# Kernel optimization log

Hardware: AMD Instinct MI355X
Metric: run time of the kernel (lower is better)

The kernel has to match this reference:

```python
import jax, jax.numpy as jnp
import numpy as np

N = 100000          # nodes per node type (paper, author)
E = 250000          # edges per relation
D_IN = 128          # input feature dim
H, C = 4, 32        # heads, channels per head (h_dim = H*C = 128)
HD = H * C
OUT = 349           # num classes
RELS = ["c", "w", "wb"]  # cites(paper->paper), writes(author->paper), written_by(paper->author)


def setup_inputs() -> dict:
    key = jax.random.key(0)
    ks = iter(jax.random.split(key, 64))
    def nrm(shape, scale=0.1):
        return jax.random.normal(next(ks), shape, jnp.float32) * scale
    inp = {
        "x_paper": jax.random.normal(next(ks), (N, D_IN), jnp.float32),
        "x_author": jax.random.normal(next(ks), (N, D_IN), jnp.float32),
        "ei_cites": jax.random.randint(next(ks), (2, E), 0, N),
        "ei_writes": jax.random.randint(next(ks), (2, E), 0, N),
        "ei_written": jax.random.randint(next(ks), (2, E), 0, N),
    }
    for l, din in [(0, D_IN), (1, HD)]:
        for r in RELS:
            inp[f"W{l}_{r}"] = nrm((din, HD))
            inp[f"as{l}_{r}"] = nrm((H, C))
            inp[f"ad{l}_{r}"] = nrm((H, C))
            inp[f"b{l}_{r}"] = jnp.zeros((HD,), jnp.float32)
    inp["lin_W"] = nrm((HD, OUT))
    inp["lin_b"] = jnp.zeros((OUT,), jnp.float32)
    return inp


def _gat_conv(x_src, x_dst, ei, W, att_s, att_d, b, n_dst):
    """PyG GATConv (concat heads, add_self_loops=False, shared lin for src/dst)."""
    h_s = (x_src @ W).reshape(-1, H, C)              # [Ns,H,C]
    h_d = (x_dst @ W).reshape(-1, H, C)              # [Nd,H,C]
    a_s = (h_s * att_s).sum(-1)                      # [Ns,H]
    a_d = (h_d * att_d).sum(-1)                      # [Nd,H]
    src, dst = ei[0], ei[1]
    e = jax.nn.leaky_relu(a_s[src] + a_d[dst], 0.2)  # [E,H]
    # segment softmax over incoming edges per dst node
    m = jax.ops.segment_max(e, dst, num_segments=n_dst)
    m = jnp.where(jnp.isfinite(m), m, 0.0)
    w = jnp.exp(e - m[dst])
    z = jax.ops.segment_sum(w, dst, num_segments=n_dst)
    alpha = w / (z[dst] + 1e-16)                     # [E,H]
    msg = h_s[src] * alpha[..., None]                # [E,H,C]
    agg = jax.ops.segment_sum(msg, dst, num_segments=n_dst)
    return agg.reshape(n_dst, HD) + b


def _forward(x_paper, x_author, ei_cites, ei_writes, ei_written, params, lin_W, lin_b):
    xp, xa = x_paper, x_author
    for l in range(2):
        p = params[l]
        # HeteroConv with sum aggregation across relations per dst node type
        op = _gat_conv(xp, xp, ei_cites, *p["c"], N) + _gat_conv(xa, xp, ei_writes, *p["w"], N)
        oa = _gat_conv(xp, xa, ei_written, *p["wb"], N)
        xp, xa = op, oa
        if l != 1:
            xp = jax.nn.leaky_relu(xp, 0.01)  # F.leaky_relu default slope
            xa = jax.nn.leaky_relu(xa, 0.01)
            # dropout: identity in eval/reference mode
    return xp @ lin_W + lin_b  # [N, OUT]


def reference(x_paper, x_author,
              W0_c, as0_c, ad0_c, b0_c, W0_w, as0_w, ad0_w, b0_w, W0_wb, as0_wb, ad0_wb, b0_wb,
              W1_c, as1_c, ad1_c, b1_c, W1_w, as1_w, ad1_w, b1_w, W1_wb, as1_wb, ad1_wb, b1_wb,
              lin_W, lin_b, ei_cites, ei_writes, ei_written):
    params = [
        {"c": (W0_c, as0_c, ad0_c, b0_c), "w": (W0_w, as0_w, ad0_w, b0_w), "wb": (W0_wb, as0_wb, ad0_wb, b0_wb)},
        {"c": (W1_c, as1_c, ad1_c, b1_c), "w": (W1_w, as1_w, ad1_w, b1_w), "wb": (W1_wb, as1_wb, ad1_wb, b1_wb)},
    ]
    return _forward(x_paper, x_author, ei_cites, ei_writes, ei_written, params, lin_W, lin_b)
```

## Files before the change

kernel.cpp:

```cpp
#include <hip/hip_runtime.h>

#define NN 100000
#define EE 250000
#define CAP 32

typedef unsigned int u32;
typedef unsigned short ushort;
typedef __attribute__((ext_vector_type(8))) short bf16x8;
typedef __attribute__((ext_vector_type(4))) float f32x4;

__device__ __forceinline__ ushort f2bf(float x) {
    u32 u = __float_as_uint(x);
    return (ushort)((u + 0x7fffu + ((u >> 16) & 1u)) >> 16);
}
__device__ __forceinline__ float bf2f(ushort h) {
    return __uint_as_float(((u32)h) << 16);
}

__global__ __launch_bounds__(256) void gemm_att(
    const float* __restrict__ X, const float* __restrict__ W,
    const float* __restrict__ atts, const float* __restrict__ attd,
    float* __restrict__ H, float* __restrict__ aS, float* __restrict__ aD)
{
    __shared__ float sW[64 * 128];
    __shared__ float sXT[128 * 32];
    const int tid = threadIdx.x;
    const size_t r0 = (size_t)blockIdx.x * 32;

    {
        int rl = tid & 31, kg = tid >> 5;
        const float4* Xr = (const float4*)(X + (r0 + rl) * 128);
#pragma unroll
        for (int t = 0; t < 4; ++t) {
            float4 u = Xr[kg * 4 + t];
            int k = kg * 16 + t * 4;
            sXT[(k + 0) * 32 + rl] = u.x;
            sXT[(k + 1) * 32 + rl] = u.y;
            sXT[(k + 2) * 32 + rl] = u.z;
            sXT[(k + 3) * 32 + rl] = u.w;
        }
    }

    const int jg = tid & 31;
    const int rg = tid >> 5;
    float acc[4][4] = {};

    for (int kh = 0; kh < 2; ++kh) {
        __syncthreads();
        const float4* Wu = (const float4*)(W + kh * 64 * 128);
        float4* sWv = (float4*)sW;
#pragma unroll
        for (int t = 0; t < 8; ++t)
            sWv[tid + 256 * t] = Wu[tid + 256 * t];
        __syncthreads();
#pragma unroll 4
        for (int k = 0; k < 64; ++k) {
            const float4 w = ((const float4*)sW)[k * 32 + jg];
            const int kk = kh * 64 + k;
            const float4 x = ((const float4*)sXT)[kk * 8 + rg];
            acc[0][0] += w.x * x.x; acc[0][1] += w.y * x.x; acc[0][2] += w.z * x.x; acc[0][3] += w.w * x.x;
            acc[1][0] += w.x * x.y; acc[1][1] += w.y * x.y; acc[1][2] += w.z * x.y; acc[1][3] += w.w * x.y;
            acc[2][0] += w.x * x.z; acc[2][1] += w.y * x.z; acc[2][2] += w.z * x.z; acc[2][3] += w.w * x.z;
            acc[3][0] += w.x * x.w; acc[3][1] += w.y * x.w; acc[3][2] += w.z * x.w; acc[3][3] += w.w * x.w;
        }
    }

    const float4 sv = ((const float4*)atts)[jg];
    const float4 dv = ((const float4*)attd)[jg];
    const int h = jg >> 3;

#pragma unroll
    for (int i = 0; i < 4; ++i) {
        const size_t row = r0 + rg * 4 + i;
        if (H)
            ((float4*)H)[row * 32 + jg] = make_float4(acc[i][0], acc[i][1], acc[i][2], acc[i][3]);
        float ps = acc[i][0] * sv.x + acc[i][1] * sv.y + acc[i][2] * sv.z + acc[i][3] * sv.w;
        float pd = acc[i][0] * dv.x + acc[i][1] * dv.y + acc[i][2] * dv.z + acc[i][3] * dv.w;
        ps += __shfl_xor(ps, 1); ps += __shfl_xor(ps, 2); ps += __shfl_xor(ps, 4);
        pd += __shfl_xor(pd, 1); pd += __shfl_xor(pd, 2); pd += __shfl_xor(pd, 4);
        if ((jg & 7) == 0) {
            aS[row * 4 + h] = ps;
            aD[row * 4 + h] = pd;
        }
    }
}

__global__ __launch_bounds__(256) void fold_w3(
    const float* __restrict__ W0, const float* __restrict__ a0,
    const float* __restrict__ W1, const float* __restrict__ a1,
    const float* __restrict__ W2, const float* __restrict__ a2,
    float* __restrict__ Wf)
{
    int i = blockIdx.x * 256 + threadIdx.x;
    if (i >= 1536) return;
    int r = i >> 9, j = i & 511;
    int k = j >> 2, h = j & 3;
    const float* W = (r == 0) ? W0 : (r == 1) ? W1 : W2;
    const float* a = (r == 0) ? a0 : (r == 1) ? a1 : a2;
    float s = 0.f;
#pragma unroll
    for (int c = 0; c < 32; ++c)
        s += W[k * 128 + h * 32 + c] * a[h * 32 + c];
    Wf[i] = s;
}

__global__ __launch_bounds__(256) void gemv_att(
    const float* __restrict__ X, const float* __restrict__ Wf,
    float* __restrict__ aD)
{
    __shared__ float sWf[512];
    const int tid = threadIdx.x;
    if (tid < 128)
        ((float4*)sWf)[tid] = ((const float4*)Wf)[tid];
    __syncthreads();
    const int t = blockIdx.x * 256 + tid;
    const int n = t >> 5, lane = t & 31;
    if (n >= NN) return;
    const float4 x = ((const float4*)X)[(size_t)n * 32 + lane];
    const float4 w0 = ((const float4*)sWf)[lane * 4 + 0];
    const float4 w1 = ((const float4*)sWf)[lane * 4 + 1];
    const float4 w2 = ((const float4*)sWf)[lane * 4 + 2];
    const float4 w3 = ((const float4*)sWf)[lane * 4 + 3];
    float p0 = x.x * w0.x + x.y * w1.x + x.z * w2.x + x.w * w3.x;
    float p1 = x.x * w0.y + x.y * w1.y + x.z * w2.y + x.w * w3.y;
    float p2 = x.x * w0.z + x.y * w1.z + x.z * w2.z + x.w * w3.z;
    float p3 = x.x * w0.w + x.y * w1.w + x.z * w2.w + x.w * w3.w;
#pragma unroll
    for (int off = 1; off < 32; off <<= 1) {
        p0 += __shfl_xor(p0, off);
        p1 += __shfl_xor(p1, off);
        p2 += __shfl_xor(p2, off);
        p3 += __shfl_xor(p3, off);
    }
    if (lane == 0)
        ((float4*)aD)[n] = make_float4(p0, p1, p2, p3);
}

__global__ __launch_bounds__(256) void fill_buckets(
    const int* __restrict__ ei, int* __restrict__ deg, int* __restrict__ bkt)
{
    int e = blockIdx.x * 256 + threadIdx.x;
    if (e >= EE) return;
    int s = ei[e], d = ei[EE + e];
    int slot = atomicAdd(&deg[d], 1);
    if (slot >= 0 && slot < CAP) bkt[(size_t)d * CAP + slot] = s;
}

__device__ __forceinline__ float4 agg_one(
    int d, int lane, int h,
    const int* __restrict__ deg, const int* __restrict__ bkt,
    const float* __restrict__ aS, const float* __restrict__ aD,
    const float* __restrict__ Hs)
{
    int g = deg[d]; if (g > CAP) g = CAP; if (g < 0) g = 0;
    const float adh = aD[d * 4 + h];
    const int* mybkt = bkt + (size_t)d * CAP;

    const int4 sa = *(const int4*)mybkt;
    const int4 sb = *(const int4*)(mybkt + 4);
    int sidx[8] = {sa.x, sa.y, sa.z, sa.w, sb.x, sb.y, sb.z, sb.w};
#pragma unroll
    for (int j = 0; j < 8; ++j)
        sidx[j] = (j < g) ? sidx[j] : 0;

    float e[8];
#pragma unroll
    for (int j = 0; j < 8; ++j) {
        float ev = aS[sidx[j] * 4 + h] + adh;
        e[j] = ev > 0.f ? ev : 0.2f * ev;
    }
    float m = -INFINITY;
#pragma unroll
    for (int j = 0; j < 8; ++j)
        if (j < g) m = fmaxf(m, e[j]);
    for (int j = 8; j < g; ++j) {
        int s = mybkt[j];
        float ev = aS[s * 4 + h] + adh;
        ev = ev > 0.f ? ev : 0.2f * ev;
        m = fmaxf(m, ev);
    }

    float4 acc = make_float4(0.f, 0.f, 0.f, 0.f);
    float z = 0.f;
#pragma unroll
    for (int j = 0; j < 8; ++j) {
        if (j < g) {
            float w = __expf(e[j] - m);
            z += w;
            float4 hv = ((const float4*)Hs)[(size_t)sidx[j] * 32 + lane];
            acc.x += w * hv.x; acc.y += w * hv.y; acc.z += w * hv.z; acc.w += w * hv.w;
        }
    }
    for (int j = 8; j < g; ++j) {
        int s = mybkt[j];
        float ev = aS[s * 4 + h] + adh;
        ev = ev > 0.f ? ev : 0.2f * ev;
        float w = __expf(ev - m);
        z += w;
        float4 hv = ((const float4*)Hs)[(size_t)s * 32 + lane];
        acc.x += w * hv.x; acc.y += w * hv.y; acc.z += w * hv.z; acc.w += w * hv.w;
    }
    float inv = 1.f / (z + 1e-16f);
    acc.x *= inv; acc.y *= inv; acc.z *= inv; acc.w *= inv;
    return acc;
}

__global__ __launch_bounds__(256) void aggregate(
    const int* __restrict__ deg, const int* __restrict__ bkt,
    const float* __restrict__ aS, const float* __restrict__ aD,
    const float* __restrict__ Hs, float* __restrict__ out,
    const float* __restrict__ b1, int act)
{
    int t = blockIdx.x * 256 + threadIdx.x;
    int d = t >> 5, lane = t & 31;
    if (d >= NN) return;
    const int h = lane >> 3;
    float4 acc = agg_one(d, lane, h, deg, bkt, aS, aD, Hs);
    if (b1) {
        float4 bv = ((const float4*)b1)[lane];
        acc.x += bv.x; acc.y += bv.y; acc.z += bv.z; acc.w += bv.w;
    }
    if (act) {
        acc.x = acc.x > 0.f ? acc.x : 0.01f * acc.x;
        acc.y = acc.y > 0.f ? acc.y : 0.01f * acc.y;
        acc.z = acc.z > 0.f ? acc.z : 0.01f * acc.z;
        acc.w = acc.w > 0.f ? acc.w : 0.01f * acc.w;
    }
    ((float4*)out)[(size_t)d * 32 + lane] = acc;
}

__global__ __launch_bounds__(256) void aggregate2(
    const int* __restrict__ deg_c, const int* __restrict__ bkt_c,
    const float* __restrict__ aS_c, const float* __restrict__ aD_c,
    const float* __restrict__ Hs_c,
    const int* __restrict__ deg_w, const int* __restrict__ bkt_w,
    const float* __restrict__ aS_w, const float* __restrict__ aD_w,
    const float* __restrict__ Hs_w,
    float* __restrict__ out,
    const float* __restrict__ b1, const float* __restrict__ b2, int act)
{
    int t = blockIdx.x * 256 + threadIdx.x;
    int d = t >> 5, lane = t & 31;
    if (d >= NN) return;
    const int h = lane >> 3;
    float4 acc_c = agg_one(d, lane, h, deg_c, bkt_c, aS_c, aD_c, Hs_c);
    float4 acc  = agg_one(d, lane, h, deg_w, bkt_w, aS_w, aD_w, Hs_w);
    acc.x += acc_c.x; acc.y += acc_c.y; acc.z += acc_c.z; acc.w += acc_c.w;
    {
        float4 bv = ((const float4*)b1)[lane];
        acc.x += bv.x; acc.y += bv.y; acc.z += bv.z; acc.w += bv.w;
    }
    {
        float4 bv = ((const float4*)b2)[lane];
        acc.x += bv.x; acc.y += bv.y; acc.z += bv.z; acc.w += bv.w;
    }
    if (act) {
        acc.x = acc.x > 0.f ? acc.x : 0.01f * acc.x;
        acc.y = acc.y > 0.f ? acc.y : 0.01f * acc.y;
        acc.z = acc.z > 0.f ? acc.z : 0.01f * acc.z;
        acc.w = acc.w > 0.f ? acc.w : 0.01f * acc.w;
    }
    ((float4*)out)[(size_t)d * 32 + lane] = acc;
}

__global__ __launch_bounds__(256) void pad_w(
    const float* __restrict__ Wl, const float* __restrict__ bl,
    ushort* __restrict__ Whi, ushort* __restrict__ Wlo, float* __restrict__ bp)
{
    int i = blockIdx.x * 256 + threadIdx.x;
    if (i >= 384 * 128) return;
    int n = i >> 7, k = i & 127;
    float w = (n < 349) ? Wl[k * 349 + n] : 0.0f;
    ushort h = f2bf(w);
    Whi[i] = h;
    Wlo[i] = f2bf(w - bf2f(h));
    if (i < 384) bp[i] = (i < 349) ? bl[i] : 0.0f;
}

__global__ __launch_bounds__(256) void gemm_out(
    const float* __restrict__ X, const ushort* __restrict__ Whi,
    const ushort* __restrict__ Wlo, const float* __restrict__ bp,
    float* __restrict__ out)
{
    __shared__ __align__(16) char smem[22400];
    ushort* sAhi = (ushort*)smem;
    ushort* sAlo = (ushort*)(smem + 8192);
    float*  sOut = (float*)smem;
    const int tid = threadIdx.x;
    const size_t r0 = (size_t)blockIdx.x * 32;

    {
        const int rl = tid >> 3, sub = tid & 7;
        const float4* Xr = (const float4*)(X + (r0 + rl) * 128);
        const u32 swz = ((u32)(rl & 7)) << 4;
#pragma unroll
        for (int i = 0; i < 2; ++i) {
            float4 u0 = Xr[sub * 4 + 2 * i];
            float4 u1 = Xr[sub * 4 + 2 * i + 1];
            float v[8] = {u0.x, u0.y, u0.z, u0.w, u1.x, u1.y, u1.z, u1.w};
            bf16x8 h8, l8;
#pragma unroll
            for (int e = 0; e < 8; ++e) {
                ushort h = f2bf(v[e]);
                h8[e] = (short)h;
                l8[e] = (short)f2bf(v[e] - bf2f(h));
            }
            u32 byteoff = (((u32)rl * 256u) + (u32)(sub * 32 + i * 16)) ^ swz;
            *(bf16x8*)((char*)sAhi + byteoff) = h8;
            *(bf16x8*)((char*)sAlo + byteoff) = l8;
        }
    }
    __syncthreads();

    const int wave = tid >> 6, lane = tid & 63;
    const int lr = lane & 15;
    const int lg = lane >> 4;
    const int ncol0 = wave * 96;

    f32x4 acc[2][6];
#pragma unroll
    for (int mt = 0; mt < 2; ++mt)
#pragma unroll
        for (int nt = 0; nt < 6; ++nt)
            acc[mt][nt] = (f32x4){0.f, 0.f, 0.f, 0.f};

    for (int ks = 0; ks < 4; ++ks) {
        bf16x8 ah[2], al[2];
#pragma unroll
        for (int mt = 0; mt < 2; ++mt) {
            const int row = mt * 16 + lr;
            u32 byteoff = (((u32)row * 256u) + (u32)(ks * 64 + lg * 16))
                          ^ (((u32)(row & 7)) << 4);
            ah[mt] = *(const bf16x8*)((const char*)sAhi + byteoff);
            al[mt] = *(const bf16x8*)((const char*)sAlo + byteoff);
        }
#pragma unroll
        for (int nt = 0; nt < 6; ++nt) {
            const int n = ncol0 + nt * 16 + lr;
            const size_t off = (size_t)n * 128 + ks * 32 + lg * 8;
            const bf16x8 bh = *(const bf16x8*)(Whi + off);
            const bf16x8 bl = *(const bf16x8*)(Wlo + off);
#pragma unroll
            for (int mt = 0; mt < 2; ++mt) {
                acc[mt][nt] = __builtin_amdgcn_mfma_f32_16x16x32_bf16(
                    ah[mt], bh, acc[mt][nt], 0, 0, 0);
                acc[mt][nt] = __builtin_amdgcn_mfma_f32_16x16x32_bf16(
                    ah[mt], bl, acc[mt][nt], 0, 0, 0);
                acc[mt][nt] = __builtin_amdgcn_mfma_f32_16x16x32_bf16(
                    al[mt], bh, acc[mt][nt], 0, 0, 0);
            }
        }
    }
    __syncthreads();

    for (int mt = 0; mt < 2; ++mt) {
        if (mt) __syncthreads();
#pragma unroll
        for (int nt = 0; nt < 6; ++nt) {
            const int n = ncol0 + nt * 16 + lr;
            if (n < 349) {
                const float bb = bp[n];
#pragma unroll
                for (int r = 0; r < 4; ++r)
                    sOut[(lg * 4 + r) * 349 + n] = acc[mt][nt][r] + bb;
            }
        }
        __syncthreads();
        {
            float4* dst = (float4*)(out + (r0 + (size_t)mt * 16) * 349);
            const float4* src = (const float4*)sOut;
            for (int i = tid; i < 1396; i += 256)
                dst[i] = src[i];
        }
    }
}

extern "C" void kernel_launch(void* const* d_in, const int* in_sizes, int n_in,
                              void* d_out, int out_size, void* d_ws, size_t ws_size,
                              hipStream_t stream)
{
    (void)in_sizes; (void)n_in; (void)out_size; (void)ws_size;
    const float* xp = (const float*)d_in[0];
    const float* xa = (const float*)d_in[1];
    const int* eic = (const int*)d_in[2];
    const int* eiw = (const int*)d_in[3];
    const int* eiwb = (const int*)d_in[4];
    auto Wl = [&](int l, int r) { return (const float*)d_in[5 + (l * 3 + r) * 4 + 0]; };
    auto As = [&](int l, int r) { return (const float*)d_in[5 + (l * 3 + r) * 4 + 1]; };
    auto Ad = [&](int l, int r) { return (const float*)d_in[5 + (l * 3 + r) * 4 + 2]; };
    auto Bs = [&](int l, int r) { return (const float*)d_in[5 + (l * 3 + r) * 4 + 3]; };
    const float* linW = (const float*)d_in[29];
    const float* linb = (const float*)d_in[30];

    char* wsp = (char*)d_ws;
    auto carve = [&](size_t bytes) -> void* {
        void* p = (void*)wsp;
        wsp += (bytes + 255) & ~(size_t)255;
        return p;
    };
    float* Hs = (float*)carve((size_t)NN * 128 * 4);
    float* P1 = (float*)carve((size_t)NN * 128 * 4);
    float* A1 = (float*)carve((size_t)NN * 128 * 4);
    float* P2 = (float*)carve((size_t)NN * 128 * 4);
    int* deg = (int*)carve((size_t)NN * 3 * 4);
    int* deg_c = deg, *deg_w = deg + NN, *deg_wb = deg + 2 * NN;
    int* bkt_c = (int*)carve((size_t)NN * CAP * 4);
    int* bkt_w = (int*)carve((size_t)NN * CAP * 4);
    int* bkt_wb = (int*)carve((size_t)NN * CAP * 4);
    float* aS = (float*)carve((size_t)NN * 4 * 4);
    float* aD = (float*)carve((size_t)NN * 4 * 4);
    float* aS2 = (float*)carve((size_t)NN * 4 * 4);
    float* aD2 = (float*)carve((size_t)NN * 4 * 4);
    float* aX = (float*)carve((size_t)NN * 4 * 4);
    ushort* Whi = (ushort*)carve((size_t)384 * 128 * 2);
    ushort* Wlo = (ushort*)carve((size_t)384 * 128 * 2);
    float* bp = (float*)carve((size_t)384 * 4);
    float* Wf = (float*)carve((size_t)3 * 512 * 4);

    dim3 blk(256);
    const int gG = NN / 32;
    const int gE = (EE + 255) / 256;
    const int gA = NN * 32 / 256;

    hipMemsetAsync(deg, 0, (size_t)NN * 3 * 4, stream);
    fill_buckets<<<gE, blk, 0, stream>>>(eic, deg_c, bkt_c);
    fill_buckets<<<gE, blk, 0, stream>>>(eiw, deg_w, bkt_w);
    fill_buckets<<<gE, blk, 0, stream>>>(eiwb, deg_wb, bkt_wb);
    fold_w3<<<6, blk, 0, stream>>>(Wl(0, 2), Ad(0, 2), Wl(0, 1), Ad(0, 1),
                                   Wl(1, 1), Ad(1, 1), Wf);

    gemm_att<<<gG, blk, 0, stream>>>(xp, Wl(0, 2), As(0, 2), Ad(0, 2), Hs, aS, aX);
    gemv_att<<<gA, blk, 0, stream>>>(xa, Wf + 0 * 512, aD);
    aggregate<<<gA, blk, 0, stream>>>(deg_wb, bkt_wb, aS, aD, Hs, A1, Bs(0, 2), 1);

    gemm_att<<<gG, blk, 0, stream>>>(xp, Wl(0, 0), As(0, 0), Ad(0, 0), Hs, aS, aD);
    gemm_att<<<gG, blk, 0, stream>>>(xa, Wl(0, 1), As(0, 1), Ad(0, 1), P2, aS2, aX);
    gemv_att<<<gA, blk, 0, stream>>>(xp, Wf + 1 * 512, aD2);
    aggregate2<<<gA, blk, 0, stream>>>(deg_c, bkt_c, aS, aD, Hs,
                                       deg_w, bkt_w, aS2, aD2, P2,
                                       P1, Bs(0, 0), Bs(0, 1), 1);

    gemm_att<<<gG, blk, 0, stream>>>(P1, Wl(1, 0), As(1, 0), Ad(1, 0), Hs, aS, aD);
    gemm_att<<<gG, blk, 0, stream>>>(A1, Wl(1, 1), As(1, 1), Ad(1, 1), A1, aS2, aX);
    gemv_att<<<gA, blk, 0, stream>>>(P1, Wf + 2 * 512, aD2);
    aggregate2<<<gA, blk, 0, stream>>>(deg_c, bkt_c, aS, aD, Hs,
                                       deg_w, bkt_w, aS2, aD2, A1,
                                       P2, Bs(1, 0), Bs(1, 1), 0);

    pad_w<<<192, blk, 0, stream>>>(linW, linb, Whi, Wlo, bp);
    gemm_out<<<gG, blk, 0, stream>>>(P2, Whi, Wlo, bp, (float*)d_out);
}
```

Measured before the change: 879.9 us.

## Move node-feature GEMMs to split-bf16 MFMA with prepacked transposed weights

```diff
diff --git a/kernel.cpp b/kernel.cpp
--- a/kernel.cpp
+++ b/kernel.cpp
@@ -17,70 +17,117 @@
     return __uint_as_float(((u32)h) << 16);
 }
 
+__global__ __launch_bounds__(256) void prep_w5(
+    const float* __restrict__ W0, const float* __restrict__ W1,
+    const float* __restrict__ W2, const float* __restrict__ W3,
+    const float* __restrict__ W4,
+    ushort* __restrict__ Whi, ushort* __restrict__ Wlo)
+{
+    int i = blockIdx.x * 256 + threadIdx.x;
+    if (i >= 5 * 16384) return;
+    int r = i >> 14, j = i & 16383;
+    int n = j >> 7, k = j & 127;
+    const float* W = (r == 0) ? W0 : (r == 1) ? W1 : (r == 2) ? W2
+                   : (r == 3) ? W3 : W4;
+    float w = W[k * 128 + n];
+    ushort h = f2bf(w);
+    Whi[i] = h;
+    Wlo[i] = f2bf(w - bf2f(h));
+}
+
 __global__ __launch_bounds__(256) void gemm_att(
-    const float* __restrict__ X, const float* __restrict__ W,
-    const float* __restrict__ atts, const float* __restrict__ attd,
-    float* __restrict__ H, float* __restrict__ aS, float* __restrict__ aD)
-{
-    __shared__ float sW[64 * 128];
-    __shared__ float sXT[128 * 32];
+    const float* __restrict__ X, const ushort* __restrict__ Whi,
+    const ushort* __restrict__ Wlo, const float* __restrict__ atts,
+    const float* __restrict__ attd, float* __restrict__ H,
+    float* __restrict__ aS, float* __restrict__ aD)
+{
+    __shared__ ushort sAhi[32 * 128];
+    __shared__ ushort sAlo[32 * 128];
     const int tid = threadIdx.x;
     const size_t r0 = (size_t)blockIdx.x * 32;
 
     {
-        int rl = tid & 31, kg = tid >> 5;
+        const int rl = tid >> 3, sub = tid & 7;
         const float4* Xr = (const float4*)(X + (r0 + rl) * 128);
-#pragma unroll
-        for (int t = 0; t < 4; ++t) {
-            float4 u = Xr[kg * 4 + t];
-            int k = kg * 16 + t * 4;
-            sXT[(k + 0) * 32 + rl] = u.x;
-            sXT[(k + 1) * 32 + rl] = u.y;
-            sXT[(k + 2) * 32 + rl] = u.z;
-            sXT[(k + 3) * 32 + rl] = u.w;
-        }
-    }
-
-    const int jg = tid & 31;
-    const int rg = tid >> 5;
-    float acc[4][4] = {};
-
-    for (int kh = 0; kh < 2; ++kh) {
-        __syncthreads();
-        const float4* Wu = (const float4*)(W + kh * 64 * 128);
-        float4* sWv = (float4*)sW;
-#pragma unroll
-        for (int t = 0; t < 8; ++t)
-            sWv[tid + 256 * t] = Wu[tid + 256 * t];
-        __syncthreads();
-#pragma unroll 4
-        for (int k = 0; k < 64; ++k) {
-            const float4 w = ((const float4*)sW)[k * 32 + jg];
-            const int kk = kh * 64 + k;
-            const float4 x = ((const float4*)sXT)[kk * 8 + rg];
-            acc[0][0] += w.x * x.x; acc[0][1] += w.y * x.x; acc[0][2] += w.z * x.x; acc[0][3] += w.w * x.x;
-            acc[1][0] += w.x * x.y; acc[1][1] += w.y * x.y; acc[1][2] += w.z * x.y; acc[1][3] += w.w * x.y;
-            acc[2][0] += w.x * x.z; acc[2][1] += w.y * x.z; acc[2][2] += w.z * x.z; acc[2][3] += w.w * x.z;
-            acc[3][0] += w.x * x.w; acc[3][1] += w.y * x.w; acc[3][2] += w.z * x.w; acc[3][3] += w.w * x.w;
-        }
-    }
-
-    const float4 sv = ((const float4*)atts)[jg];
-    const float4 dv = ((const float4*)attd)[jg];
-    const int h = jg >> 3;
-
-#pragma unroll
-    for (int i = 0; i < 4; ++i) {
-        const size_t row = r0 + rg * 4 + i;
-        if (H)
-            ((float4*)H)[row * 32 + jg] = make_float4(acc[i][0], acc[i][1], acc[i][2], acc[i][3]);
-        float ps = acc[i][0] * sv.x + acc[i][1] * sv.y + acc[i][2] * sv.z + acc[i][3] * sv.w;
-        float pd = acc[i][0] * dv.x + acc[i][1] * dv.y + acc[i][2] * dv.z + acc[i][3] * dv.w;
-        ps += __shfl_xor(ps, 1); ps += __shfl_xor(ps, 2); ps += __shfl_xor(ps, 4);
-        pd += __shfl_xor(pd, 1); pd += __shfl_xor(pd, 2); pd += __shfl_xor(pd, 4);
-        if ((jg & 7) == 0) {
-            aS[row * 4 + h] = ps;
-            aD[row * 4 + h] = pd;
+        const u32 swz = ((u32)(rl & 7)) << 4;
+#pragma unroll
+        for (int i = 0; i < 2; ++i) {
+            float4 u0 = Xr[sub * 4 + 2 * i];
+            float4 u1 = Xr[sub * 4 + 2 * i + 1];
+            float v[8] = {u0.x, u0.y, u0.z, u0.w, u1.x, u1.y, u1.z, u1.w};
+            bf16x8 h8, l8;
+#pragma unroll
+            for (int e = 0; e < 8; ++e) {
+                ushort h = f2bf(v[e]);
+                h8[e] = (short)h;
+                l8[e] = (short)f2bf(v[e] - bf2f(h));
+            }
+            u32 byteoff = (((u32)rl * 256u) + (u32)(sub * 32 + i * 16)) ^ swz;
+            *(bf16x8*)((char*)sAhi + byteoff) = h8;
+            *(bf16x8*)((char*)sAlo + byteoff) = l8;
+        }
+    }
+    __syncthreads();
+
+    const int wave = tid >> 6, lane = tid & 63;
+    const int lr = lane & 15;
+    const int lg = lane >> 4;
+    const int ncol0 = wave * 32;
+
+    f32x4 acc[2][2];
+#pragma unroll
+    for (int mt = 0; mt < 2; ++mt)
+#pragma unroll
+        for (int nt = 0; nt < 2; ++nt)
+            acc[mt][nt] = (f32x4){0.f, 0.f, 0.f, 0.f};
+
+    for (int ks = 0; ks < 4; ++ks) {
+        bf16x8 ah[2], al[2];
+#pragma unroll
+        for (int mt = 0; mt < 2; ++mt) {
+            const int row = mt * 16 + lr;
+            u32 byteoff = (((u32)row * 256u) + (u32)(ks * 64 + lg * 16))
+                          ^ (((u32)(row & 7)) << 4);
+            ah[mt] = *(const bf16x8*)((const char*)sAhi + byteoff);
+            al[mt] = *(const bf16x8*)((const char*)sAlo + byteoff);
+        }
+#pragma unroll
+        for (int nt = 0; nt < 2; ++nt) {
+            const int n = ncol0 + nt * 16 + lr;
+            const size_t off = (size_t)n * 128 + ks * 32 + lg * 8;
+            const bf16x8 bh = *(const bf16x8*)(Whi + off);
+            const bf16x8 bl = *(const bf16x8*)(Wlo + off);
+#pragma unroll
+            for (int mt = 0; mt < 2; ++mt) {
+                acc[mt][nt] = __builtin_amdgcn_mfma_f32_16x16x32_bf16(
+                    ah[mt], bh, acc[mt][nt], 0, 0, 0);
+                acc[mt][nt] = __builtin_amdgcn_mfma_f32_16x16x32_bf16(
+                    ah[mt], bl, acc[mt][nt], 0, 0, 0);
+                acc[mt][nt] = __builtin_amdgcn_mfma_f32_16x16x32_bf16(
+                    al[mt], bh, acc[mt][nt], 0, 0, 0);
+            }
+        }
+    }
+
+    const float sv0 = atts[ncol0 + lr],      sv1 = atts[ncol0 + 16 + lr];
+    const float dv0 = attd[ncol0 + lr],      dv1 = attd[ncol0 + 16 + lr];
+#pragma unroll
+    for (int mt = 0; mt < 2; ++mt) {
+#pragma unroll
+        for (int r = 0; r < 4; ++r) {
+            const size_t grow = r0 + mt * 16 + lg * 4 + r;
+            H[grow * 128 + ncol0 + lr]      = acc[mt][0][r];
+            H[grow * 128 + ncol0 + 16 + lr] = acc[mt][1][r];
+            float ps = acc[mt][0][r] * sv0 + acc[mt][1][r] * sv1;
+            float pd = acc[mt][0][r] * dv0 + acc[mt][1][r] * dv1;
+            ps += __shfl_xor(ps, 1); ps += __shfl_xor(ps, 2);
+            ps += __shfl_xor(ps, 4); ps += __shfl_xor(ps, 8);
+            pd += __shfl_xor(pd, 1); pd += __shfl_xor(pd, 2);
+            pd += __shfl_xor(pd, 4); pd += __shfl_xor(pd, 8);
+            if (lr == 0) {
+                aS[grow * 4 + wave] = ps;
+                aD[grow * 4 + wave] = pd;
+            }
         }
     }
 }
@@ -367,10 +414,9 @@
         }
         __syncthreads();
         {
-            float4* dst = (float4*)(out + (r0 + (size_t)mt * 16) * 349);
-            const float4* src = (const float4*)sOut;
-            for (int i = tid; i < 1396; i += 256)
-                dst[i] = src[i];
+            float* dst = out + (r0 + (size_t)mt * 16) * 349;
+            for (int i = tid; i < 5584; i += 256)
+                dst[i] = sOut[i];
         }
     }
 }
@@ -416,6 +462,8 @@
     ushort* Wlo = (ushort*)carve((size_t)384 * 128 * 2);
     float* bp = (float*)carve((size_t)384 * 4);
     float* Wf = (float*)carve((size_t)3 * 512 * 4);
+    ushort* Whi5 = (ushort*)carve((size_t)5 * 16384 * 2);
+    ushort* Wlo5 = (ushort*)carve((size_t)5 * 16384 * 2);
 
     dim3 blk(256);
     const int gG = NN / 32;
@@ -428,20 +476,27 @@
     fill_buckets<<<gE, blk, 0, stream>>>(eiwb, deg_wb, bkt_wb);
     fold_w3<<<6, blk, 0, stream>>>(Wl(0, 2), Ad(0, 2), Wl(0, 1), Ad(0, 1),
                                    Wl(1, 1), Ad(1, 1), Wf);
-
-    gemm_att<<<gG, blk, 0, stream>>>(xp, Wl(0, 2), As(0, 2), Ad(0, 2), Hs, aS, aX);
+    prep_w5<<<320, blk, 0, stream>>>(Wl(0, 2), Wl(0, 0), Wl(0, 1),
+                                     Wl(1, 0), Wl(1, 1), Whi5, Wlo5);
+
+    gemm_att<<<gG, blk, 0, stream>>>(xp, Whi5 + 0 * 16384, Wlo5 + 0 * 16384,
+                                     As(0, 2), Ad(0, 2), Hs, aS, aX);
     gemv_att<<<gA, blk, 0, stream>>>(xa, Wf + 0 * 512, aD);
     aggregate<<<gA, blk, 0, stream>>>(deg_wb, bkt_wb, aS, aD, Hs, A1, Bs(0, 2), 1);
 
-    gemm_att<<<gG, blk, 0, stream>>>(xp, Wl(0, 0), As(0, 0), Ad(0, 0), Hs, aS, aD);
-    gemm_att<<<gG, blk, 0, stream>>>(xa, Wl(0, 1), As(0, 1), Ad(0, 1), P2, aS2, aX);
+    gemm_att<<<gG, blk, 0, stream>>>(xp, Whi5 + 1 * 16384, Wlo5 + 1 * 16384,
+                                     As(0, 0), Ad(0, 0), Hs, aS, aD);
+    gemm_att<<<gG, blk, 0, stream>>>(xa, Whi5 + 2 * 16384, Wlo5 + 2 * 16384,
+                                     As(0, 1), Ad(0, 1), P2, aS2, aX);
     gemv_att<<<gA, blk, 0, stream>>>(xp, Wf + 1 * 512, aD2);
     aggregate2<<<gA, blk, 0, stream>>>(deg_c, bkt_c, aS, aD, Hs,
                                        deg_w, bkt_w, aS2, aD2, P2,
                                        P1, Bs(0, 0), Bs(0, 1), 1);
 
-    gemm_att<<<gG, blk, 0, stream>>>(P1, Wl(1, 0), As(1, 0), Ad(1, 0), Hs, aS, aD);
-    gemm_att<<<gG, blk, 0, stream>>>(A1, Wl(1, 1), As(1, 1), Ad(1, 1), A1, aS2, aX);
+    gemm_att<<<gG, blk, 0, stream>>>(P1, Whi5 + 3 * 16384, Wlo5 + 3 * 16384,
+                                     As(1, 0), Ad(1, 0), Hs, aS, aD);
+    gemm_att<<<gG, blk, 0, stream>>>(A1, Whi5 + 4 * 16384, Wlo5 + 4 * 16384,
+                                     As(1, 1), Ad(1, 1), A1, aS2, aX);
     gemv_att<<<gA, blk, 0, stream>>>(P1, Wf + 2 * 512, aD2);
     aggregate2<<<gA, blk, 0, stream>>>(deg_c, bkt_c, aS, aD, Hs,
                                        deg_w, bkt_w, aS2, aD2, A1,
```

Result: faster. 822.8 us (-6.5%).
